# Optimization experiments

Measured on AMD Instinct MI355X. Metric: run time of the kernel, lower is better.

The kernel has to match this reference:

```python
import jax, jax.numpy as jnp
import numpy as np

DIM = 2048
N_HEADS = 16
N_KV_HEADS = 4
HEAD_DIM = DIM // N_HEADS  # 128
N_REP = N_HEADS // N_KV_HEADS  # 4
BASE = 10000.0


def rotate_half(x):
    x1, x2 = jnp.split(x, 2, axis=-1)
    return jnp.concatenate((-x2, x1), axis=-1)


def rope_cos_sin(seq_len, dtype):
    inv_freq = 1.0 / (BASE ** (jnp.arange(0, HEAD_DIM, 2, dtype=jnp.float32) / HEAD_DIM))
    t = jnp.arange(seq_len, dtype=jnp.float32)
    freqs = jnp.outer(t, inv_freq)                      # [T, hd/2]
    emb = jnp.concatenate((freqs, freqs), axis=-1)      # [T, hd]
    return jnp.cos(emb).astype(dtype), jnp.sin(emb).astype(dtype)


def setup_inputs() -> dict:
    key = jax.random.key(0)
    ks = jax.random.split(key, 5)
    B, T = 2, 2048
    s_in = 1.0 / np.sqrt(DIM)
    x = jax.random.normal(ks[0], (B, T, DIM), dtype=jnp.float32)
    wq = jax.random.normal(ks[1], (DIM, N_HEADS * HEAD_DIM), dtype=jnp.float32) * s_in
    wk = jax.random.normal(ks[2], (DIM, N_KV_HEADS * HEAD_DIM), dtype=jnp.float32) * s_in
    wv = jax.random.normal(ks[3], (DIM, N_KV_HEADS * HEAD_DIM), dtype=jnp.float32) * s_in
    wo = jax.random.normal(ks[4], (DIM, DIM), dtype=jnp.float32) * s_in
    return {"x": x, "wq": wq, "wk": wk, "wv": wv, "wo": wo}


def reference(x, wq, wk, wv, wo):
    B, T, D = x.shape
    scale = HEAD_DIM ** -0.5
    # projections -> [B, H, T, hd]
    q = (x @ wq).reshape(B, T, N_HEADS, HEAD_DIM).transpose(0, 2, 1, 3)
    k = (x @ wk).reshape(B, T, N_KV_HEADS, HEAD_DIM).transpose(0, 2, 1, 3)
    v = (x @ wv).reshape(B, T, N_KV_HEADS, HEAD_DIM).transpose(0, 2, 1, 3)
    # RoPE
    cos, sin = rope_cos_sin(T, x.dtype)  # [T, hd]
    q = q * cos + rotate_half(q) * sin
    k = k * cos + rotate_half(k) * sin
    # GQA: group queries by kv head instead of repeating K/V
    qg = q.reshape(B, N_KV_HEADS, N_REP, T, HEAD_DIM)
    attn = jnp.einsum('bgrqd,bgkd->bgrqk', qg, k) * scale  # [B, G, R, T, T]
    causal = jnp.tril(jnp.ones((T, T), dtype=bool))
    attn = jnp.where(causal, attn, jnp.finfo(attn.dtype).min)
    attn = jax.nn.softmax(attn, axis=-1)
    out = jnp.einsum('bgrqk,bgkd->bgrqd', attn, v)  # [B, G, R, T, hd]
    out = out.reshape(B, N_HEADS, T, HEAD_DIM).transpose(0, 2, 1, 3).reshape(B, T, D)
    return out @ wo
```

## Files before the change

kernel.cpp:

```cpp
#include <hip/hip_runtime.h>
#include <hip/hip_bf16.h>

#define DIM 2048
#define T_SEQ 2048
#define B_SZ 2
#define NH 16
#define NKV 4
#define HD 128
#define KVDIM (NKV * HD)
#define M_ROWS (B_SZ * T_SEQ)
#define QKVN (DIM + 2 * KVDIM)
#define QBLK 128
#define KVBLK 64

typedef float f32x4 __attribute__((ext_vector_type(4)));
typedef __bf16 bf16x8 __attribute__((ext_vector_type(8)));
typedef unsigned short u16x8 __attribute__((ext_vector_type(8)));

static __device__ __forceinline__ float bf2f(unsigned short u) {
    unsigned v = ((unsigned)u) << 16;
    return __builtin_bit_cast(float, v);
}
static __device__ __forceinline__ unsigned short f2bf(float f) {
    __bf16 h = (__bf16)f;
    return __builtin_bit_cast(unsigned short, h);
}

static __device__ __forceinline__ void gload16(const void* g, void* l) {
    __builtin_amdgcn_global_load_lds((const __attribute__((address_space(1))) void*)g,
                                     (__attribute__((address_space(3))) void*)l, 16, 0, 0);
}

__global__ void cvt_f32_bf16(const float* __restrict__ src, unsigned short* __restrict__ dst, int n4) {
    int i = blockIdx.x * blockDim.x + threadIdx.x;
    if (i >= n4) return;
    float4 v = ((const float4*)src)[i];
    ushort4 o;
    o.x = f2bf(v.x); o.y = f2bf(v.y); o.z = f2bf(v.z); o.w = f2bf(v.w);
    ((ushort4*)dst)[i] = o;
}

__global__ void build_tab(float2* __restrict__ tab) {
    const int idx = blockIdx.x * 256 + threadIdx.x;
    if (idx >= T_SEQ * 64) return;
    const int tt = idx >> 6, i = idx & 63;
    const float inv = exp2f(-(float)i * (13.287712379549449f / 64.0f));
    const float ang = (float)tt * inv;
    tab[idx] = make_float2(cosf(ang), sinf(ang));
}

__global__ void transpose_w(const float* __restrict__ wq, const float* __restrict__ wk,
                            const float* __restrict__ wv, const float* __restrict__ wo,
                            unsigned short* __restrict__ wqkvT, unsigned short* __restrict__ woT) {
    __shared__ float tl[32][33];
    const int tx = threadIdx.x, ty = threadIdx.y;
    const int n0 = blockIdx.x * 32, k0 = blockIdx.y * 32;
    const float* src;
    unsigned short* dstbase;
    int N, nn;
    if (n0 < DIM) { src = wq; N = DIM; nn = n0; dstbase = wqkvT + (size_t)n0 * DIM; }
    else if (n0 < DIM + KVDIM) { src = wk; N = KVDIM; nn = n0 - DIM; dstbase = wqkvT + (size_t)n0 * DIM; }
    else if (n0 < QKVN) { src = wv; N = KVDIM; nn = n0 - DIM - KVDIM; dstbase = wqkvT + (size_t)n0 * DIM; }
    else { src = wo; N = DIM; nn = n0 - QKVN; dstbase = woT + (size_t)(n0 - QKVN) * DIM; }
#pragma unroll
    for (int i = 0; i < 4; ++i)
        tl[ty + i * 8][tx] = src[(size_t)(k0 + ty + i * 8) * N + nn + tx];
    __syncthreads();
#pragma unroll
    for (int i = 0; i < 4; ++i)
        dstbase[(size_t)(ty + i * 8) * DIM + k0 + tx] = f2bf(tl[tx][ty + i * 8]);
}

__global__ void transpose_v(const unsigned short* __restrict__ qkv, unsigned short* __restrict__ Vt) {
    __shared__ unsigned short tl[32][33];
    const int t0 = blockIdx.x * 32;
    const int d0 = blockIdx.y * 32;
    const int bg = blockIdx.z;
    const int b = bg >> 2, g = bg & 3;
    unsigned short* dst = Vt + (size_t)bg * T_SEQ * HD;
    const int tx = threadIdx.x, ty = threadIdx.y;
#pragma unroll
    for (int i = 0; i < 4; ++i)
        tl[ty + i * 8][tx] = qkv[((size_t)(b * T_SEQ) + t0 + ty + i * 8) * QKVN +
                                 (DIM + KVDIM) + g * HD + d0 + tx];
    __syncthreads();
#pragma unroll
    for (int i = 0; i < 4; ++i)
        dst[(size_t)(d0 + ty + i * 8) * T_SEQ + t0 + tx] = tl[tx][ty + i * 8];
}

static __device__ __forceinline__ void store_out(float* p, float v) { *p = v; }
static __device__ __forceinline__ void store_out(unsigned short* p, float v) { *p = f2bf(v); }

template <typename OutT>
__global__ __launch_bounds__(512, 2) void gemm8(const unsigned short* __restrict__ A,
                                                const unsigned short* __restrict__ BT,
                                                OutT* __restrict__ C, int M, int N, int K, int Ntiles) {
    __shared__ __align__(16) unsigned short ldsA[2][2][256 * 32];
    __shared__ __align__(16) unsigned short ldsB[2][2][256 * 32];
    const int nwg = gridDim.x;
    const int f = blockIdx.x;
    const int swz = (f & 7) * (nwg >> 3) + (f >> 3);
    const int m0 = (swz / Ntiles) * 256, n0 = (swz % Ntiles) * 256;
    const int t = threadIdx.x;
    const int lane = t & 63, w = t >> 6;
    const int wr = w >> 2, wc = w & 3;
    const int grp = lane >> 4, c = lane & 15;
    const int nkt = K >> 6;

    const int Rs = t >> 2;
    const int cbs = ((t & 3) * 16) ^ ((Rs & 8) << 2);
    const char* Ag = (const char*)A + (size_t)(m0 + Rs) * (K * 2) + cbs;
    const char* Bg = (const char*)BT + (size_t)(n0 + Rs) * (K * 2) + cbs;
    const size_t rowstep = (size_t)128 * K * 2;

    auto stage = [&](int buf, int mat, int ks, int kt) {
        const char* g0 = (mat ? Bg : Ag) + kt * 128 + ks * 64;
        char* l = (mat ? (char*)&ldsB[buf][ks][0] : (char*)&ldsA[buf][ks][0]) + t * 16;
        gload16(g0, l);
        gload16(g0 + rowstep, l + 512 * 16);
    };
    auto rdA = [&](int buf, int ks, int fr) {
        const int R = wr * 128 + fr * 16 + c;
        return *(const bf16x8*)((const char*)&ldsA[buf][ks][0] + R * 64 + ((grp * 16) ^ ((R & 8) << 2)));
    };
    auto rdB = [&](int buf, int ks, int fc) {
        const int R = wc * 64 + fc * 16 + c;
        return *(const bf16x8*)((const char*)&ldsB[buf][ks][0] + R * 64 + ((grp * 16) ^ ((R & 8) << 2)));
    };

    f32x4 acc[8][4] = {};
    bf16x8 aF[8], bF0, bF1;

    stage(0, 0, 0, 0); stage(0, 1, 0, 0); stage(0, 0, 1, 0); stage(0, 1, 1, 0);
    stage(1, 0, 0, 1); stage(1, 1, 0, 1);
    asm volatile("s_waitcnt vmcnt(4)" ::: "memory");
    asm volatile("s_barrier" ::: "memory");

    for (int kt = 0; kt < nkt; ++kt) {
        const int buf = kt & 1;
#pragma unroll
        for (int fr = 0; fr < 8; ++fr) aF[fr] = rdA(buf, 0, fr);
        bF0 = rdB(buf, 0, 0); bF1 = rdB(buf, 0, 1);
        if (kt + 1 < nkt) stage(buf ^ 1, 0, 1, kt + 1);
        asm volatile("s_barrier" ::: "memory");
        __builtin_amdgcn_s_setprio(1);
#pragma unroll
        for (int fr = 0; fr < 8; ++fr) {
            acc[fr][0] = __builtin_amdgcn_mfma_f32_16x16x32_bf16(aF[fr], bF0, acc[fr][0], 0, 0, 0);
            acc[fr][1] = __builtin_amdgcn_mfma_f32_16x16x32_bf16(aF[fr], bF1, acc[fr][1], 0, 0, 0);
        }
        __builtin_amdgcn_s_setprio(0);
        asm volatile("s_barrier" ::: "memory");
        bF0 = rdB(buf, 0, 2); bF1 = rdB(buf, 0, 3);
        if (kt + 1 < nkt) stage(buf ^ 1, 1, 1, kt + 1);
        asm volatile("s_barrier" ::: "memory");
        __builtin_amdgcn_s_setprio(1);
#pragma unroll
        for (int fr = 0; fr < 8; ++fr) {
            acc[fr][2] = __builtin_amdgcn_mfma_f32_16x16x32_bf16(aF[fr], bF0, acc[fr][2], 0, 0, 0);
            acc[fr][3] = __builtin_amdgcn_mfma_f32_16x16x32_bf16(aF[fr], bF1, acc[fr][3], 0, 0, 0);
        }
        __builtin_amdgcn_s_setprio(0);
        asm volatile("s_barrier" ::: "memory");
#pragma unroll
        for (int fr = 0; fr < 8; ++fr) aF[fr] = rdA(buf, 1, fr);
        bF0 = rdB(buf, 1, 0); bF1 = rdB(buf, 1, 1);
        if (kt + 2 < nkt) stage(buf, 0, 0, kt + 2);
        asm volatile("s_barrier" ::: "memory");
        __builtin_amdgcn_s_setprio(1);
#pragma unroll
        for (int fr = 0; fr < 8; ++fr) {
            acc[fr][0] = __builtin_amdgcn_mfma_f32_16x16x32_bf16(aF[fr], bF0, acc[fr][0], 0, 0, 0);
            acc[fr][1] = __builtin_amdgcn_mfma_f32_16x16x32_bf16(aF[fr], bF1, acc[fr][1], 0, 0, 0);
        }
        __builtin_amdgcn_s_setprio(0);
        asm volatile("s_barrier" ::: "memory");
        bF0 = rdB(buf, 1, 2); bF1 = rdB(buf, 1, 3);
        if (kt + 2 < nkt) stage(buf, 1, 0, kt + 2);
        asm volatile("s_barrier" ::: "memory");
        __builtin_amdgcn_s_setprio(1);
#pragma unroll
        for (int fr = 0; fr < 8; ++fr) {
            acc[fr][2] = __builtin_amdgcn_mfma_f32_16x16x32_bf16(aF[fr], bF0, acc[fr][2], 0, 0, 0);
            acc[fr][3] = __builtin_amdgcn_mfma_f32_16x16x32_bf16(aF[fr], bF1, acc[fr][3], 0, 0, 0);
        }
        __builtin_amdgcn_s_setprio(0);
        asm volatile("s_waitcnt vmcnt(4)" ::: "memory");
        asm volatile("s_barrier" ::: "memory");
    }
#pragma unroll
    for (int fr = 0; fr < 8; ++fr)
#pragma unroll
        for (int fc = 0; fc < 4; ++fc)
#pragma unroll
            for (int rr = 0; rr < 4; ++rr) {
                const int row = m0 + wr * 128 + fr * 16 + grp * 4 + rr;
                const int col = n0 + wc * 64 + fc * 16 + c;
                store_out(&C[(size_t)row * N + col], acc[fr][fc][rr]);
            }
}

template <typename OutT>
__global__ __launch_bounds__(512, 1) void gemmwo(const unsigned short* __restrict__ A,
                                                 const unsigned short* __restrict__ BT,
                                                 OutT* __restrict__ C, int M, int N, int K, int Ntiles) {
    __shared__ __align__(16) unsigned short ldsA[2][2][256 * 32];
    __shared__ __align__(16) unsigned short ldsB[2][2][128 * 32];
    const int nwg = gridDim.x;
    const int f = blockIdx.x;
    const int swz = (f & 7) * (nwg >> 3) + (f >> 3);
    const int m0 = (swz / Ntiles) * 256, n0 = (swz % Ntiles) * 128;
    const int t = threadIdx.x;
    const int lane = t & 63, w = t >> 6;
    const int wr = w >> 2, wc = w & 3;
    const int grp = lane >> 4, c = lane & 15;
    const int nkt = K >> 6;

    const int Rs = t >> 2;
    const int cbs = ((t & 3) * 16) ^ ((Rs & 8) << 2);
    const char* Ag = (const char*)A + (size_t)(m0 + Rs) * (K * 2) + cbs;
    const char* Bg = (const char*)BT + (size_t)(n0 + Rs) * (K * 2) + cbs;
    const size_t rowstep = (size_t)128 * K * 2;

    auto stageA = [&](int buf, int ks, int kt) {
        const char* g0 = Ag + kt * 128 + ks * 64;
        char* l = (char*)&ldsA[buf][ks][0] + t * 16;
        gload16(g0, l);
        gload16(g0 + rowstep, l + 512 * 16);
    };
    auto stageB = [&](int buf, int ks, int kt) {
        gload16(Bg + kt * 128 + ks * 64, (char*)&ldsB[buf][ks][0] + t * 16);
    };
    auto rdA = [&](int buf, int ks, int fr) {
        const int R = wr * 128 + fr * 16 + c;
        return *(const bf16x8*)((const char*)&ldsA[buf][ks][0] + R * 64 + ((grp * 16) ^ ((R & 8) << 2)));
    };
    auto rdB = [&](int buf, int ks, int fc) {
        const int R = wc * 32 + fc * 16 + c;
        return *(const bf16x8*)((const char*)&ldsB[buf][ks][0] + R * 64 + ((grp * 16) ^ ((R & 8) << 2)));
    };

    f32x4 acc[8][2] = {};
    bf16x8 aF[8], bF0, bF1;

    stageA(0, 0, 0); stageB(0, 0, 0); stageA(0, 1, 0); stageB(0, 1, 0);
    stageA(1, 0, 1); stageB(1, 0, 1);
    asm volatile("s_waitcnt vmcnt(3)" ::: "memory");
    asm volatile("s_barrier" ::: "memory");

    for (int kt = 0; kt < nkt; ++kt) {
        const int buf = kt & 1;
#pragma unroll
        for (int fr = 0; fr < 8; ++fr) aF[fr] = rdA(buf, 0, fr);
        bF0 = rdB(buf, 0, 0); bF1 = rdB(buf, 0, 1);
        if (kt + 1 < nkt) { stageA(buf ^ 1, 1, kt + 1); stageB(buf ^ 1, 1, kt + 1); }
        asm volatile("s_barrier" ::: "memory");
        __builtin_amdgcn_s_setprio(1);
#pragma unroll
        for (int fr = 0; fr < 8; ++fr) {
            acc[fr][0] = __builtin_amdgcn_mfma_f32_16x16x32_bf16(aF[fr], bF0, acc[fr][0], 0, 0, 0);
            acc[fr][1] = __builtin_amdgcn_mfma_f32_16x16x32_bf16(aF[fr], bF1, acc[fr][1], 0, 0, 0);
        }
        __builtin_amdgcn_s_setprio(0);
        asm volatile("s_barrier" ::: "memory");
#pragma unroll
        for (int fr = 0; fr < 8; ++fr) aF[fr] = rdA(buf, 1, fr);
        bF0 = rdB(buf, 1, 0); bF1 = rdB(buf, 1, 1);
        if (kt + 2 < nkt) { stageA(buf, 0, kt + 2); stageB(buf, 0, kt + 2); }
        asm volatile("s_barrier" ::: "memory");
        __builtin_amdgcn_s_setprio(1);
#pragma unroll
        for (int fr = 0; fr < 8; ++fr) {
            acc[fr][0] = __builtin_amdgcn_mfma_f32_16x16x32_bf16(aF[fr], bF0, acc[fr][0], 0, 0, 0);
            acc[fr][1] = __builtin_amdgcn_mfma_f32_16x16x32_bf16(aF[fr], bF1, acc[fr][1], 0, 0, 0);
        }
        __builtin_amdgcn_s_setprio(0);
        if (kt + 2 < nkt) { asm volatile("s_waitcnt vmcnt(3)" ::: "memory"); }
        else              { asm volatile("s_waitcnt vmcnt(0)" ::: "memory"); }
        asm volatile("s_barrier" ::: "memory");
    }
#pragma unroll
    for (int fr = 0; fr < 8; ++fr)
#pragma unroll
        for (int fc = 0; fc < 2; ++fc)
#pragma unroll
            for (int rr = 0; rr < 4; ++rr) {
                const int row = m0 + wr * 128 + fr * 16 + grp * 4 + rr;
                const int col = n0 + wc * 32 + fc * 16 + c;
                store_out(&C[(size_t)row * N + col], acc[fr][fc][rr]);
            }
}

__global__ __launch_bounds__(256) void rope_pack(const unsigned short* __restrict__ qkv,
                                                 const float2* __restrict__ tab,
                                                 unsigned short* __restrict__ Qb,
                                                 unsigned short* __restrict__ Kb) {
    const int bt = blockIdx.x;
    const int b = bt >> 11, tt = bt & 2047;
    __shared__ float cs[64], sn[64];
    const int tid = threadIdx.x;
    if (tid < 64) {
        float2 v = tab[tt * 64 + tid];
        cs[tid] = v.x;
        sn[tid] = v.y;
    }
    __syncthreads();
    const float qscale = 0.08838834764831845f * 1.4426950408889634f;
    const size_t src0 = (size_t)bt * QKVN;
#pragma unroll
    for (int iter = 0; iter < 4; ++iter) {
        const int idx = iter * 256 + tid;
        const int h = idx >> 6, i = idx & 63;
        const size_t src = src0 + h * HD;
        const float x1 = bf2f(qkv[src + i]), x2 = bf2f(qkv[src + i + 64]);
        const size_t dst = (((size_t)(b * NH + h)) * T_SEQ + tt) * HD;
        Qb[dst + i] = f2bf((x1 * cs[i] - x2 * sn[i]) * qscale);
        Qb[dst + i + 64] = f2bf((x2 * cs[i] + x1 * sn[i]) * qscale);
    }
    {
        const int gg = tid >> 6, i = tid & 63;
        const size_t src = src0 + DIM + gg * HD;
        const float x1 = bf2f(qkv[src + i]), x2 = bf2f(qkv[src + i + 64]);
        const size_t dst = (((size_t)(b * NKV + gg)) * T_SEQ + tt) * HD;
        Kb[dst + i] = f2bf(x1 * cs[i] - x2 * sn[i]);
        Kb[dst + i + 64] = f2bf(x2 * cs[i] + x1 * sn[i]);
    }
}

__global__ __launch_bounds__(512, 4) void attn_kernel(const unsigned short* __restrict__ Qb,
                                                      const unsigned short* __restrict__ Kb,
                                                      const unsigned short* __restrict__ Vt,
                                                      unsigned short* __restrict__ Ob) {
    __shared__ __align__(16) unsigned short Kl[2][KVBLK * HD];
    __shared__ __align__(16) unsigned short Vl[2][HD * KVBLK];
    const int bid = blockIdx.x;
    const int bh = bid & 31;
    const int qt = (T_SEQ / QBLK - 1) - (bid >> 5);
    const int b = bh >> 4, h = bh & 15;
    const int g = h >> 2;
    const int t = threadIdx.x, lane = t & 63, w = t >> 6;
    const int grp = lane >> 4, c = lane & 15;
    const int q0 = qt * QBLK;
    const int wq = q0 + w * 16;

    bf16x8 qf[4];
    {
        const size_t qbase = ((size_t)(b * NH + h) * T_SEQ + wq + c) * HD;
#pragma unroll
        for (int kk = 0; kk < 4; ++kk)
            qf[kk] = *(const bf16x8*)(Qb + qbase + kk * 32 + grp * 8);
    }
    const size_t kbase = (size_t)(b * NKV + g) * T_SEQ * HD;

    const char* kp[2];
    const char* vp[2];
#pragma unroll
    for (int i = 0; i < 2; ++i) {
        const int s = (i * 512 + t) * 16;
        const int rl = s >> 8, csw = s & 255;
        const int col = csw ^ ((rl & 7) << 4);
        const int rl32 = rl & 31;
        const int kvrow = (rl >> 5) * 32 + ((rl32 >> 2) & 3) * 8 + ((rl32 >> 4) & 1) * 4 + (rl32 & 3);
        kp[i] = (const char*)(Kb + kbase) + kvrow * (HD * 2) + col;
        const int d = s >> 7, csw2 = s & 127;
        const int kvb = csw2 ^ ((d & 7) << 4);
        vp[i] = (const char*)(Vt + kbase) + (size_t)d * (T_SEQ * 2) + kvb;
    }

    f32x4 o[8] = {};
    float l_run = 0.f;
    const int nkv = (q0 + QBLK) / KVBLK;

#pragma unroll
    for (int i = 0; i < 2; ++i) {
        gload16(kp[i], (char*)Kl[0] + (i * 512 + t) * 16);
        gload16(vp[i], (char*)Vl[0] + (i * 512 + t) * 16);
    }

    for (int kt = 0; kt < nkv; ++kt) {
        const int cur = kt & 1;
        __syncthreads();
        if (kt + 1 < nkv) {
#pragma unroll
            for (int i = 0; i < 2; ++i) {
                gload16(kp[i] + (size_t)(kt + 1) * (KVBLK * HD * 2), (char*)Kl[cur ^ 1] + (i * 512 + t) * 16);
                gload16(vp[i] + (size_t)(kt + 1) * (KVBLK * 2), (char*)Vl[cur ^ 1] + (i * 512 + t) * 16);
            }
        }
        const int kv0 = kt * KVBLK;
        if (kv0 > wq + 15) continue;
        f32x4 s4[4] = {};
        __builtin_amdgcn_s_setprio(1);
#pragma unroll
        for (int kvc = 0; kvc < 4; ++kvc) {
            const int row = kvc * 16 + c;
            bf16x8 kf[4];
#pragma unroll
            for (int kk = 0; kk < 4; ++kk)
                kf[kk] = *(const bf16x8*)((const char*)Kl[cur] + row * 256 +
                                          ((kk * 64 + grp * 16) ^ ((row & 7) << 4)));
#pragma unroll
            for (int kk = 0; kk < 4; ++kk)
                s4[kvc] = __builtin_amdgcn_mfma_f32_16x16x32_bf16(kf[kk], qf[kk], s4[kvc], 0, 0, 0);
        }
        __builtin_amdgcn_s_setprio(0);
        bf16x8 pb[2];
        if (kv0 + KVBLK - 1 > wq) {
#pragma unroll
            for (int kvc = 0; kvc < 4; ++kvc)
#pragma unroll
                for (int r = 0; r < 4; ++r) {
                    const int kvg = kv0 + (kvc >> 1) * 32 + grp * 8 + (kvc & 1) * 4 + r;
                    if (kvg > wq + c) s4[kvc][r] = -1e30f;
                }
        }
        float ls = 0.f;
#pragma unroll
        for (int kvc = 0; kvc < 4; ++kvc)
#pragma unroll
            for (int r = 0; r < 4; ++r) {
                const float pv = exp2f(s4[kvc][r]);
                pb[kvc >> 1][(kvc & 1) * 4 + r] = (__bf16)pv;
                ls += pv;
            }
        l_run += ls;
        __builtin_amdgcn_s_setprio(1);
#pragma unroll
        for (int ch = 0; ch < 2; ++ch) {
#pragma unroll
            for (int dt = 0; dt < 8; ++dt) {
                const int d = dt * 16 + c;
                const bf16x8 vf = *(const bf16x8*)((const char*)Vl[cur] + d * 128 +
                                                   ((ch * 64 + grp * 16) ^ ((d & 7) << 4)));
                o[dt] = __builtin_amdgcn_mfma_f32_16x16x32_bf16(pb[ch], vf, o[dt], 0, 0, 0);
            }
        }
        __builtin_amdgcn_s_setprio(0);
    }
    {
        float ls = l_run;
        ls += __shfl_xor(ls, 16);
        ls += __shfl_xor(ls, 32);
        float lo[4];
#pragma unroll
        for (int r = 0; r < 4; ++r) lo[r] = 1.0f / __shfl(ls, grp * 4 + r);
#pragma unroll
        for (int dt = 0; dt < 8; ++dt)
#pragma unroll
            for (int r = 0; r < 4; ++r) {
                const int trow = wq + grp * 4 + r;
                Ob[((size_t)(b * T_SEQ) + trow) * DIM + h * HD + dt * 16 + c] = f2bf(o[dt][r] * lo[r]);
            }
    }
}

extern "C" void kernel_launch(void* const* d_in, const int* in_sizes, int n_in,
                              void* d_out, int out_size, void* d_ws, size_t ws_size,
                              hipStream_t stream) {
    const float* x = (const float*)d_in[0];
    const float* wq = (const float*)d_in[1];
    const float* wk = (const float*)d_in[2];
    const float* wv = (const float*)d_in[3];
    const float* wo = (const float*)d_in[4];
    float* out = (float*)d_out;

    char* ws = (char*)d_ws;
    size_t off = 0;
    auto alloc = [&](size_t bytes) {
        char* p = ws + off;
        off = (off + bytes + 255) & ~(size_t)255;
        return p;
    };
    unsigned short* xb    = (unsigned short*)alloc((size_t)M_ROWS * DIM * 2);
    unsigned short* wqkvT = (unsigned short*)alloc((size_t)QKVN * DIM * 2);
    unsigned short* woT   = (unsigned short*)alloc((size_t)DIM * DIM * 2);
    unsigned short* qkv   = (unsigned short*)alloc((size_t)M_ROWS * QKVN * 2);
    unsigned short* Kb    = (unsigned short*)alloc((size_t)M_ROWS * KVDIM * 2);
    float2*         tab   = (float2*)alloc((size_t)T_SEQ * 64 * sizeof(float2));
    unsigned short* Qb    = xb;
    unsigned short* Vt    = wqkvT;
    unsigned short* attnO = qkv;

    cvt_f32_bf16<<<(M_ROWS * DIM / 4 + 255) / 256, 256, 0, stream>>>(x, xb, M_ROWS * DIM / 4);
    build_tab<<<(T_SEQ * 64 + 255) / 256, 256, 0, stream>>>(tab);

    dim3 tb(32, 8);
    transpose_w<<<dim3((QKVN + DIM) / 32, DIM / 32), tb, 0, stream>>>(wq, wk, wv, wo, wqkvT, woT);

    gemm8<unsigned short><<<(M_ROWS / 256) * (QKVN / 256), 512, 0, stream>>>(xb, wqkvT, qkv, M_ROWS, QKVN, DIM, QKVN / 256);

    rope_pack<<<M_ROWS, 256, 0, stream>>>(qkv, tab, Qb, Kb);
    transpose_v<<<dim3(T_SEQ / 32, HD / 32, B_SZ * NKV), tb, 0, stream>>>(qkv, Vt);

    attn_kernel<<<(B_SZ * NH) * (T_SEQ / QBLK), 512, 0, stream>>>(Qb, Kb, Vt, attnO);

    gemmwo<float><<<(M_ROWS / 256) * (DIM / 128), 512, 0, stream>>>(attnO, woT, out, M_ROWS, DIM, DIM, DIM / 128);
}
```

Before: 204.0 us.

## Split attention warps into 32-row query by 64-dim output tiles

Each wave now owns 32 query rows and half of the head dimension instead of 16 rows and the full dimension. A K fragment read from LDS feeds two QK MFMAs and each V fragment feeds two PV MFMAs, halving LDS reads per MFMA in the PV stage. The trade-off is that QK^T and the softmax exp for a row pair are computed twice, once by each of the two waves sharing those rows. That roughly doubles the QK MFMA and exp work per block, and causal skipping becomes coarser at 32-row granularity.

```diff
diff --git a/kernel.cpp b/kernel.cpp
--- a/kernel.cpp
+++ b/kernel.cpp
@@ -340,16 +340,18 @@
     const int b = bh >> 4, h = bh & 15;
     const int g = h >> 2;
     const int t = threadIdx.x, lane = t & 63, w = t >> 6;
+    const int wqg = w >> 1, dg = w & 1;
     const int grp = lane >> 4, c = lane & 15;
     const int q0 = qt * QBLK;
-    const int wq = q0 + w * 16;
-
-    bf16x8 qf[4];
-    {
-        const size_t qbase = ((size_t)(b * NH + h) * T_SEQ + wq + c) * HD;
+    const int qw = q0 + wqg * 32;
+
+    bf16x8 qf[2][4];
+#pragma unroll
+    for (int qi = 0; qi < 2; ++qi) {
+        const size_t qbase = ((size_t)(b * NH + h) * T_SEQ + qw + qi * 16 + c) * HD;
 #pragma unroll
         for (int kk = 0; kk < 4; ++kk)
-            qf[kk] = *(const bf16x8*)(Qb + qbase + kk * 32 + grp * 8);
+            qf[qi][kk] = *(const bf16x8*)(Qb + qbase + kk * 32 + grp * 8);
     }
     const size_t kbase = (size_t)(b * NKV + g) * T_SEQ * HD;
 
@@ -368,8 +370,8 @@
         vp[i] = (const char*)(Vt + kbase) + (size_t)d * (T_SEQ * 2) + kvb;
     }
 
-    f32x4 o[8] = {};
-    float l_run = 0.f;
+    f32x4 o[2][4] = {};
+    float l_run[2] = {0.f, 0.f};
     const int nkv = (q0 + QBLK) / KVBLK;
 
 #pragma unroll
@@ -389,8 +391,8 @@
             }
         }
         const int kv0 = kt * KVBLK;
-        if (kv0 > wq + 15) continue;
-        f32x4 s4[4] = {};
+        if (kv0 > qw + 31) continue;
+        f32x4 s[2][4] = {};
         __builtin_amdgcn_s_setprio(1);
 #pragma unroll
         for (int kvc = 0; kvc < 4; ++kvc) {
@@ -401,56 +403,65 @@
                 kf[kk] = *(const bf16x8*)((const char*)Kl[cur] + row * 256 +
                                           ((kk * 64 + grp * 16) ^ ((row & 7) << 4)));
 #pragma unroll
-            for (int kk = 0; kk < 4; ++kk)
-                s4[kvc] = __builtin_amdgcn_mfma_f32_16x16x32_bf16(kf[kk], qf[kk], s4[kvc], 0, 0, 0);
-        }
-        __builtin_amdgcn_s_setprio(0);
-        bf16x8 pb[2];
-        if (kv0 + KVBLK - 1 > wq) {
+            for (int kk = 0; kk < 4; ++kk) {
+                s[0][kvc] = __builtin_amdgcn_mfma_f32_16x16x32_bf16(kf[kk], qf[0][kk], s[0][kvc], 0, 0, 0);
+                s[1][kvc] = __builtin_amdgcn_mfma_f32_16x16x32_bf16(kf[kk], qf[1][kk], s[1][kvc], 0, 0, 0);
+            }
+        }
+        __builtin_amdgcn_s_setprio(0);
+        bf16x8 pb[2][2];
+#pragma unroll
+        for (int qi = 0; qi < 2; ++qi) {
+            const int qmin = qw + qi * 16;
+            if (kv0 + KVBLK - 1 > qmin) {
+#pragma unroll
+                for (int kvc = 0; kvc < 4; ++kvc)
+#pragma unroll
+                    for (int r = 0; r < 4; ++r) {
+                        const int kvg = kv0 + (kvc >> 1) * 32 + grp * 8 + (kvc & 1) * 4 + r;
+                        if (kvg > qmin + c) s[qi][kvc][r] = -1e30f;
+                    }
+            }
+            float ls = 0.f;
 #pragma unroll
             for (int kvc = 0; kvc < 4; ++kvc)
 #pragma unroll
                 for (int r = 0; r < 4; ++r) {
-                    const int kvg = kv0 + (kvc >> 1) * 32 + grp * 8 + (kvc & 1) * 4 + r;
-                    if (kvg > wq + c) s4[kvc][r] = -1e30f;
+                    const float pv = exp2f(s[qi][kvc][r]);
+                    pb[qi][kvc >> 1][(kvc & 1) * 4 + r] = (__bf16)pv;
+                    ls += pv;
                 }
-        }
-        float ls = 0.f;
-#pragma unroll
-        for (int kvc = 0; kvc < 4; ++kvc)
-#pragma unroll
-            for (int r = 0; r < 4; ++r) {
-                const float pv = exp2f(s4[kvc][r]);
-                pb[kvc >> 1][(kvc & 1) * 4 + r] = (__bf16)pv;
-                ls += pv;
-            }
-        l_run += ls;
+            l_run[qi] += ls;
+        }
         __builtin_amdgcn_s_setprio(1);
 #pragma unroll
         for (int ch = 0; ch < 2; ++ch) {
 #pragma unroll
-            for (int dt = 0; dt < 8; ++dt) {
-                const int d = dt * 16 + c;
+            for (int dt = 0; dt < 4; ++dt) {
+                const int d = dg * 64 + dt * 16 + c;
                 const bf16x8 vf = *(const bf16x8*)((const char*)Vl[cur] + d * 128 +
                                                    ((ch * 64 + grp * 16) ^ ((d & 7) << 4)));
-                o[dt] = __builtin_amdgcn_mfma_f32_16x16x32_bf16(pb[ch], vf, o[dt], 0, 0, 0);
-            }
-        }
-        __builtin_amdgcn_s_setprio(0);
-    }
-    {
-        float ls = l_run;
+                o[0][dt] = __builtin_amdgcn_mfma_f32_16x16x32_bf16(pb[0][ch], vf, o[0][dt], 0, 0, 0);
+                o[1][dt] = __builtin_amdgcn_mfma_f32_16x16x32_bf16(pb[1][ch], vf, o[1][dt], 0, 0, 0);
+            }
+        }
+        __builtin_amdgcn_s_setprio(0);
+    }
+#pragma unroll
+    for (int qi = 0; qi < 2; ++qi) {
+        float ls = l_run[qi];
         ls += __shfl_xor(ls, 16);
         ls += __shfl_xor(ls, 32);
         float lo[4];
 #pragma unroll
         for (int r = 0; r < 4; ++r) lo[r] = 1.0f / __shfl(ls, grp * 4 + r);
 #pragma unroll
-        for (int dt = 0; dt < 8; ++dt)
+        for (int dt = 0; dt < 4; ++dt)
 #pragma unroll
             for (int r = 0; r < 4; ++r) {
-                const int trow = wq + grp * 4 + r;
-                Ob[((size_t)(b * T_SEQ) + trow) * DIM + h * HD + dt * 16 + c] = f2bf(o[dt][r] * lo[r]);
+                const int trow = qw + qi * 16 + grp * 4 + r;
+                const int col = h * HD + dg * 64 + dt * 16 + c;
+                Ob[((size_t)(b * T_SEQ) + trow) * DIM + col] = f2bf(o[qi][dt][r] * lo[r]);
             }
     }
 }
```

After: 225.4 us. 10.5% more time.

## Fuse RoPE, Q/K packing and V transpose into the QKV GEMM epilogue

Applied to the files above, without the earlier changes.

The QKV projection GEMM now writes RoPE-rotated, scaled Q, rotated K, and transposed V directly from its accumulators. To make that possible it remaps the B-fragment columns so each wave holds matching rotate-half pairs. This removes the intermediate qkv buffer and two separate kernels (rope_pack and transpose_v), along with their extra global memory round trips and launches. The attention kernel's q-tile order also changes so that heavy and light causal tiles interleave, but the epilogue's scattered 2-byte stores may be less coalesced.

```diff
diff --git a/kernel.cpp b/kernel.cpp
--- a/kernel.cpp
+++ b/kernel.cpp
@@ -71,31 +71,16 @@
         dstbase[(size_t)(ty + i * 8) * DIM + k0 + tx] = f2bf(tl[tx][ty + i * 8]);
 }
 
-__global__ void transpose_v(const unsigned short* __restrict__ qkv, unsigned short* __restrict__ Vt) {
-    __shared__ unsigned short tl[32][33];
-    const int t0 = blockIdx.x * 32;
-    const int d0 = blockIdx.y * 32;
-    const int bg = blockIdx.z;
-    const int b = bg >> 2, g = bg & 3;
-    unsigned short* dst = Vt + (size_t)bg * T_SEQ * HD;
-    const int tx = threadIdx.x, ty = threadIdx.y;
-#pragma unroll
-    for (int i = 0; i < 4; ++i)
-        tl[ty + i * 8][tx] = qkv[((size_t)(b * T_SEQ) + t0 + ty + i * 8) * QKVN +
-                                 (DIM + KVDIM) + g * HD + d0 + tx];
-    __syncthreads();
-#pragma unroll
-    for (int i = 0; i < 4; ++i)
-        dst[(size_t)(d0 + ty + i * 8) * T_SEQ + t0 + tx] = tl[tx][ty + i * 8];
-}
-
 static __device__ __forceinline__ void store_out(float* p, float v) { *p = v; }
 static __device__ __forceinline__ void store_out(unsigned short* p, float v) { *p = f2bf(v); }
 
-template <typename OutT>
-__global__ __launch_bounds__(512, 2) void gemm8(const unsigned short* __restrict__ A,
-                                                const unsigned short* __restrict__ BT,
-                                                OutT* __restrict__ C, int M, int N, int K, int Ntiles) {
+__global__ __launch_bounds__(512, 2) void gemm8_qkv(const unsigned short* __restrict__ A,
+                                                    const unsigned short* __restrict__ BT,
+                                                    const float2* __restrict__ tab,
+                                                    unsigned short* __restrict__ Qb,
+                                                    unsigned short* __restrict__ Kb,
+                                                    unsigned short* __restrict__ Vt) {
+    constexpr int K = DIM, Ntiles = QKVN / 256;
     __shared__ __align__(16) unsigned short ldsA[2][2][256 * 32];
     __shared__ __align__(16) unsigned short ldsB[2][2][256 * 32];
     const int nwg = gridDim.x;
@@ -107,6 +92,7 @@
     const int wr = w >> 2, wc = w & 3;
     const int grp = lane >> 4, c = lane & 15;
     const int nkt = K >> 6;
+    const int hloc = wc >> 1, qh = wc & 1;
 
     const int Rs = t >> 2;
     const int cbs = ((t & 3) * 16) ^ ((Rs & 8) << 2);
@@ -125,7 +111,7 @@
         return *(const bf16x8*)((const char*)&ldsA[buf][ks][0] + R * 64 + ((grp * 16) ^ ((R & 8) << 2)));
     };
     auto rdB = [&](int buf, int ks, int fc) {
-        const int R = wc * 64 + fc * 16 + c;
+        const int R = hloc * 128 + (fc >> 1) * 64 + qh * 32 + (fc & 1) * 16 + c;
         return *(const bf16x8*)((const char*)&ldsB[buf][ks][0] + R * 64 + ((grp * 16) ^ ((R & 8) << 2)));
     };
 
@@ -189,16 +175,60 @@
         asm volatile("s_waitcnt vmcnt(4)" ::: "memory");
         asm volatile("s_barrier" ::: "memory");
     }
-#pragma unroll
-    for (int fr = 0; fr < 8; ++fr)
-#pragma unroll
-        for (int fc = 0; fc < 4; ++fc)
-#pragma unroll
-            for (int rr = 0; rr < 4; ++rr) {
-                const int row = m0 + wr * 128 + fr * 16 + grp * 4 + rr;
-                const int col = n0 + wc * 64 + fc * 16 + c;
-                store_out(&C[(size_t)row * N + col], acc[fr][fc][rr]);
-            }
+    const float qscale = 0.08838834764831845f * 1.4426950408889634f;
+    if (n0 < DIM) {
+        const int h = (n0 >> 7) + hloc;
+#pragma unroll
+        for (int fi = 0; fi < 2; ++fi) {
+            const int i = qh * 32 + fi * 16 + c;
+#pragma unroll
+            for (int fr = 0; fr < 8; ++fr)
+#pragma unroll
+                for (int rr = 0; rr < 4; ++rr) {
+                    const int row = m0 + wr * 128 + fr * 16 + grp * 4 + rr;
+                    const int bb = row >> 11, tt = row & 2047;
+                    const float2 csn = tab[tt * 64 + i];
+                    const float x1 = acc[fr][fi][rr], x2 = acc[fr][2 + fi][rr];
+                    unsigned short* dst = Qb + (((size_t)(bb * NH + h)) * T_SEQ + tt) * HD;
+                    dst[i] = f2bf((x1 * csn.x - x2 * csn.y) * qscale);
+                    dst[i + 64] = f2bf((x2 * csn.x + x1 * csn.y) * qscale);
+                }
+        }
+    } else if (n0 < DIM + KVDIM) {
+        const int g = ((n0 - DIM) >> 7) + hloc;
+#pragma unroll
+        for (int fi = 0; fi < 2; ++fi) {
+            const int i = qh * 32 + fi * 16 + c;
+#pragma unroll
+            for (int fr = 0; fr < 8; ++fr)
+#pragma unroll
+                for (int rr = 0; rr < 4; ++rr) {
+                    const int row = m0 + wr * 128 + fr * 16 + grp * 4 + rr;
+                    const int bb = row >> 11, tt = row & 2047;
+                    const float2 csn = tab[tt * 64 + i];
+                    const float x1 = acc[fr][fi][rr], x2 = acc[fr][2 + fi][rr];
+                    unsigned short* dst = Kb + (((size_t)(bb * NKV + g)) * T_SEQ + tt) * HD;
+                    dst[i] = f2bf(x1 * csn.x - x2 * csn.y);
+                    dst[i + 64] = f2bf(x2 * csn.x + x1 * csn.y);
+                }
+        }
+    } else {
+        const int g = ((n0 - DIM - KVDIM) >> 7) + hloc;
+#pragma unroll
+        for (int fc = 0; fc < 4; ++fc) {
+            const int d = (fc >> 1) * 64 + qh * 32 + (fc & 1) * 16 + c;
+#pragma unroll
+            for (int fr = 0; fr < 8; ++fr) {
+                const int row0 = m0 + wr * 128 + fr * 16 + grp * 4;
+                const int bb = row0 >> 11, tt0 = row0 & 2047;
+                unsigned short* dst = Vt + (((size_t)(bb * NKV + g)) * HD + d) * T_SEQ + tt0;
+                ushort4 pk;
+                pk.x = f2bf(acc[fr][fc][0]); pk.y = f2bf(acc[fr][fc][1]);
+                pk.z = f2bf(acc[fr][fc][2]); pk.w = f2bf(acc[fr][fc][3]);
+                *(ushort4*)dst = pk;
+            }
+        }
+    }
 }
 
 template <typename OutT>
@@ -292,42 +322,6 @@
             }
 }
 
-__global__ __launch_bounds__(256) void rope_pack(const unsigned short* __restrict__ qkv,
-                                                 const float2* __restrict__ tab,
-                                                 unsigned short* __restrict__ Qb,
-                                                 unsigned short* __restrict__ Kb) {
-    const int bt = blockIdx.x;
-    const int b = bt >> 11, tt = bt & 2047;
-    __shared__ float cs[64], sn[64];
-    const int tid = threadIdx.x;
-    if (tid < 64) {
-        float2 v = tab[tt * 64 + tid];
-        cs[tid] = v.x;
-        sn[tid] = v.y;
-    }
-    __syncthreads();
-    const float qscale = 0.08838834764831845f * 1.4426950408889634f;
-    const size_t src0 = (size_t)bt * QKVN;
-#pragma unroll
-    for (int iter = 0; iter < 4; ++iter) {
-        const int idx = iter * 256 + tid;
-        const int h = idx >> 6, i = idx & 63;
-        const size_t src = src0 + h * HD;
-        const float x1 = bf2f(qkv[src + i]), x2 = bf2f(qkv[src + i + 64]);
-        const size_t dst = (((size_t)(b * NH + h)) * T_SEQ + tt) * HD;
-        Qb[dst + i] = f2bf((x1 * cs[i] - x2 * sn[i]) * qscale);
-        Qb[dst + i + 64] = f2bf((x2 * cs[i] + x1 * sn[i]) * qscale);
-    }
-    {
-        const int gg = tid >> 6, i = tid & 63;
-        const size_t src = src0 + DIM + gg * HD;
-        const float x1 = bf2f(qkv[src + i]), x2 = bf2f(qkv[src + i + 64]);
-        const size_t dst = (((size_t)(b * NKV + gg)) * T_SEQ + tt) * HD;
-        Kb[dst + i] = f2bf(x1 * cs[i] - x2 * sn[i]);
-        Kb[dst + i + 64] = f2bf(x2 * cs[i] + x1 * sn[i]);
-    }
-}
-
 __global__ __launch_bounds__(512, 4) void attn_kernel(const unsigned short* __restrict__ Qb,
                                                       const unsigned short* __restrict__ Kb,
                                                       const unsigned short* __restrict__ Vt,
@@ -336,7 +330,8 @@
     __shared__ __align__(16) unsigned short Vl[2][HD * KVBLK];
     const int bid = blockIdx.x;
     const int bh = bid & 31;
-    const int qt = (T_SEQ / QBLK - 1) - (bid >> 5);
+    const int j = bid >> 5;
+    const int qt = (j < 8) ? (15 - j) : (j - 8);
     const int b = bh >> 4, h = bh & 15;
     const int g = h >> 2;
     const int t = threadIdx.x, lane = t & 63, w = t >> 6;
@@ -475,12 +470,11 @@
     unsigned short* xb    = (unsigned short*)alloc((size_t)M_ROWS * DIM * 2);
     unsigned short* wqkvT = (unsigned short*)alloc((size_t)QKVN * DIM * 2);
     unsigned short* woT   = (unsigned short*)alloc((size_t)DIM * DIM * 2);
-    unsigned short* qkv   = (unsigned short*)alloc((size_t)M_ROWS * QKVN * 2);
+    unsigned short* Qb    = (unsigned short*)alloc((size_t)M_ROWS * DIM * 2);
     unsigned short* Kb    = (unsigned short*)alloc((size_t)M_ROWS * KVDIM * 2);
+    unsigned short* Vt    = (unsigned short*)alloc((size_t)M_ROWS * KVDIM * 2);
     float2*         tab   = (float2*)alloc((size_t)T_SEQ * 64 * sizeof(float2));
-    unsigned short* Qb    = xb;
-    unsigned short* Vt    = wqkvT;
-    unsigned short* attnO = qkv;
+    unsigned short* attnO = xb;
 
     cvt_f32_bf16<<<(M_ROWS * DIM / 4 + 255) / 256, 256, 0, stream>>>(x, xb, M_ROWS * DIM / 4);
     build_tab<<<(T_SEQ * 64 + 255) / 256, 256, 0, stream>>>(tab);
@@ -488,10 +482,7 @@
     dim3 tb(32, 8);
     transpose_w<<<dim3((QKVN + DIM) / 32, DIM / 32), tb, 0, stream>>>(wq, wk, wv, wo, wqkvT, woT);
 
-    gemm8<unsigned short><<<(M_ROWS / 256) * (QKVN / 256), 512, 0, stream>>>(xb, wqkvT, qkv, M_ROWS, QKVN, DIM, QKVN / 256);
-
-    rope_pack<<<M_ROWS, 256, 0, stream>>>(qkv, tab, Qb, Kb);
-    transpose_v<<<dim3(T_SEQ / 32, HD / 32, B_SZ * NKV), tb, 0, stream>>>(qkv, Vt);
+    gemm8_qkv<<<(M_ROWS / 256) * (QKVN / 256), 512, 0, stream>>>(xb, wqkvT, tab, Qb, Kb, Vt);
 
     attn_kernel<<<(B_SZ * NH) * (T_SEQ / QBLK), 512, 0, stream>>>(Qb, Kb, Vt, attnO);
 
```

After: 192.0 us. 1.06x faster.
